# Kernel tuning notes

Measured on AMD Instinct MI355X. Metric: run time of the kernel, lower is better.

Reference implementation:

```python
import jax, jax.numpy as jnp
import numpy as np

N, M, H = 65536, 256, 4           # memory_units, memory_unit_size, num_heads
CTRL, IN, OUT = 1024, 2048, 2048  # ctrl_dim, input_dim, output_dim
LSTM_IN = IN + H * M
EPS = 1e-8


def setup_inputs() -> dict:
    key = jax.random.key(0)
    ks = jax.random.split(key, 12)
    s = 0.02
    return {
        "x": jax.random.normal(ks[0], (1, IN), jnp.float32),
        "prev_reads": jax.random.normal(ks[1], (H, M), jnp.float32),
        "prev_h": jax.random.normal(ks[2], (1, CTRL), jnp.float32),
        "prev_c": jax.random.normal(ks[3], (1, CTRL), jnp.float32),
        "memory": jax.random.normal(ks[4], (N, M), jnp.float32) * 0.1,
        "prev_rw": jax.nn.softmax(jax.random.normal(ks[5], (H, N), jnp.float32), axis=-1),
        "prev_ww": jax.nn.softmax(jax.random.normal(ks[6], (H, N), jnp.float32), axis=-1),
        "W_ih": jax.random.normal(ks[7], (4 * CTRL, LSTM_IN), jnp.float32) * s,
        "W_hh": jax.random.normal(ks[8], (4 * CTRL, CTRL), jnp.float32) * s,
        "b_lstm": jnp.zeros((4 * CTRL,), jnp.float32),
        "W_out": jax.random.normal(ks[9], (OUT, H * M), jnp.float32) * s,
        "b_out": jnp.zeros((OUT,), jnp.float32),
        "Ww": jax.random.normal(ks[10], (H, 3 * M + 6, CTRL), jnp.float32) * s,
        "bw": jnp.zeros((H, 3 * M + 6), jnp.float32),
        "Wr": jax.random.normal(ks[11], (H, M + 6, CTRL), jnp.float32) * s,
        "br": jnp.zeros((H, M + 6), jnp.float32),
    }


def _address(o, prev_w, mem):
    # o: [M+6 or 3M+6] head fc output; prev_w: [N]; mem: [N, M]
    k = jnp.tanh(o[:M])                         # key
    beta = jax.nn.softplus(o[M])                # key strength
    g = jax.nn.sigmoid(o[M + 1])                # interpolation gate
    sft = jax.nn.softmax(o[M + 2:M + 5])        # shift weights (-1, 0, +1)
    gamma = 1.0 + jax.nn.softplus(o[M + 5])     # sharpening
    sim = (mem @ k) / (jnp.linalg.norm(mem, axis=1) * jnp.linalg.norm(k) + EPS)
    wc = jax.nn.softmax(beta * sim)             # content addressing [N]
    wg = g * wc + (1.0 - g) * prev_w            # interpolation
    ws = sft[0] * jnp.roll(wg, -1) + sft[1] * wg + sft[2] * jnp.roll(wg, 1)
    wsh = jnp.maximum(ws, 1e-12) ** gamma       # sharpen
    return wsh / (jnp.sum(wsh) + EPS)


def reference(x, prev_reads, prev_h, prev_c, memory, prev_rw, prev_ww,
              W_ih, W_hh, b_lstm, W_out, b_out, Ww, bw, Wr, br):
    # Controller LSTM cell: input = [x ; flattened previous reads]
    inp = jnp.concatenate([x, prev_reads.reshape(1, -1)], axis=-1)
    gates = inp @ W_ih.T + prev_h @ W_hh.T + b_lstm
    i_g, f_g, g_g, _ = jnp.split(gates, 4, axis=-1)
    c = jax.nn.sigmoid(f_g) * prev_c + jax.nn.sigmoid(i_g) * jnp.tanh(g_g)
    ctrl = c[0]  # heads consume the controller cell state (as in forward)
    mem = memory
    reads = []
    for hd in range(H):  # heads ordered [w0, r0, w1, r1, ...] as in the module
        ow = Ww[hd] @ ctrl + bw[hd]
        ww = _address(ow, prev_ww[hd], mem)
        e = jax.nn.sigmoid(ow[M + 6:2 * M + 6])
        a = jnp.tanh(ow[2 * M + 6:3 * M + 6])
        mem = mem * (1.0 - ww[:, None] * e[None, :]) + ww[:, None] * a[None, :]
        orr = Wr[hd] @ ctrl + br[hd]
        rw = _address(orr, prev_rw[hd], mem)
        reads.append(rw @ mem)  # [M]
    reads = jnp.stack(reads)    # [H, M]
    return reads.reshape(1, -1) @ W_out.T + b_out  # [1, OUT]
```

## Files before the change

kernel.cpp:

```cpp
#include <hip/hip_runtime.h>
#include <cmath>

#define NMEM 65536
#define MSZ  256
#define EPSC 1e-8f
#define GRID_BIG 512

enum : int {
    OFF_GATES = 0,
    OFF_CTRL  = 4096,
    OFF_OW    = 5120,
    OFF_ORR   = 8216,
    OFF_K     = 9264,
    OFF_E     = 11312,
    OFF_A     = 12336,
    OFF_SCAL  = 13360,
    OFF_READS = 13424,
    OFF_PAIRS = 14448,
    OFF_TPART = 15472,
    OFF_SIM   = 15728,
    OFF_WSH   = 81264,
    OFF_NSQ   = 146800,
    WS_FLOATS = 212336
};

__device__ __forceinline__ float wave_sum(float v) {
#pragma unroll
    for (int off = 32; off > 0; off >>= 1) v += __shfl_xor(v, off);
    return v;
}
__device__ __forceinline__ float sigmoidf_(float x) { return 1.f / (1.f + expf(-x)); }
__device__ __forceinline__ float softplusf_(float x) { return (x > 20.f) ? x : log1pf(expf(x)); }
__device__ __forceinline__ void pair_merge(float& m, float& s, float m2, float s2) {
    if (m2 > m) { s = s * expf(m - m2) + s2; m = m2; }
    else        { s += s2 * expf(m2 - m); }
}
__device__ __forceinline__ float dot4(float4 a, float4 b) {
    return a.x * b.x + a.y * b.y + a.z * b.z + a.w * b.w;
}

__device__ __forceinline__ void block_pair_out(float m, float s, float* ws,
                                               int t, int lane, int wid) {
    __shared__ float sm[4], ss2[4];
    if (lane == 0) { sm[wid] = m; ss2[wid] = s; }
    __syncthreads();
    if (t == 0) {
        float M = sm[0], S = ss2[0];
#pragma unroll
        for (int i = 1; i < 4; ++i) pair_merge(M, S, sm[i], ss2[i]);
        ws[OFF_PAIRS + blockIdx.x * 2]     = M;
        ws[OFF_PAIRS + blockIdx.x * 2 + 1] = S;
    }
}

#define BFLY8(arr)                                            \
    _Pragma("unroll")                                         \
    for (int off = 32; off > 0; off >>= 1) {                  \
        _Pragma("unroll")                                     \
        for (int r = 0; r < 8; ++r) arr[r] += __shfl_xor(arr[r], off); \
    }

__global__ __launch_bounds__(256) void k_gates(
    const float* __restrict__ x, const float* __restrict__ prev_reads,
    const float* __restrict__ prev_h, const float* __restrict__ W_ih,
    const float* __restrict__ W_hh, const float* __restrict__ b_lstm,
    float* __restrict__ ws)
{
    const int row  = (blockIdx.x * 256 + threadIdx.x) >> 6;
    const int lane = threadIdx.x & 63;
    const float* wrow = W_ih + (size_t)row * 3072;
    float acc = 0.f;
#pragma unroll
    for (int j = lane * 4; j < 3072; j += 256) {
        float4 w4 = *(const float4*)(wrow + j);
        float4 v4 = (j < 2048) ? *(const float4*)(x + j)
                               : *(const float4*)(prev_reads + (j - 2048));
        acc += dot4(w4, v4);
    }
    const float* hrow = W_hh + (size_t)row * 1024;
#pragma unroll
    for (int j = lane * 4; j < 1024; j += 256) {
        acc += dot4(*(const float4*)(hrow + j), *(const float4*)(prev_h + j));
    }
    acc = wave_sum(acc);
    if (lane == 0) ws[OFF_GATES + row] = acc + b_lstm[row];
}

__global__ void k_cell(const float* __restrict__ prev_c, float* __restrict__ ws) {
    const int j = blockIdx.x * blockDim.x + threadIdx.x;
    if (j >= 1024) return;
    const float ig = ws[OFF_GATES + j];
    const float fg = ws[OFF_GATES + 1024 + j];
    const float gg = ws[OFF_GATES + 2048 + j];
    ws[OFF_CTRL + j] = sigmoidf_(fg) * prev_c[j] + sigmoidf_(ig) * tanhf(gg);
}

__global__ __launch_bounds__(256) void k_headfc(
    const float* __restrict__ Ww, const float* __restrict__ bw,
    const float* __restrict__ Wr, const float* __restrict__ br,
    float* __restrict__ ws)
{
    const int gwv  = (blockIdx.x * 256 + threadIdx.x) >> 6;
    const int lane = threadIdx.x & 63;
    const float* wrow; float bias; int dst;
    if (gwv < 3096) { wrow = Ww + (size_t)gwv * 1024; bias = bw[gwv]; dst = OFF_OW + gwv; }
    else { const int rr = gwv - 3096; wrow = Wr + (size_t)rr * 1024; bias = br[rr]; dst = OFF_ORR + rr; }
    const float* ctrl = ws + OFF_CTRL;
    float acc = 0.f;
#pragma unroll
    for (int j = lane * 4; j < 1024; j += 256) {
        acc += dot4(*(const float4*)(wrow + j), *(const float4*)(ctrl + j));
    }
    acc = wave_sum(acc);
    if (lane == 0) ws[dst] = acc + bias;
}

__global__ __launch_bounds__(256) void k_params(float* __restrict__ ws) {
    const int p = blockIdx.x, t = threadIdx.x;
    const float* o = (p < 4) ? (ws + OFF_OW + p * 774) : (ws + OFF_ORR + (p - 4) * 262);
    const float kj = tanhf(o[t]);
    ws[OFF_K + p * 256 + t] = kj;
    float ssq = wave_sum(kj * kj);
    __shared__ float red[4];
    if ((t & 63) == 0) red[t >> 6] = ssq;
    __syncthreads();
    if (t == 0) {
        float* sc = ws + OFF_SCAL + p * 8;
        sc[0] = sqrtf(red[0] + red[1] + red[2] + red[3]);
        sc[1] = softplusf_(o[256]);
        sc[2] = sigmoidf_(o[257]);
        const float a0 = o[258], a1 = o[259], a2 = o[260];
        const float mm = fmaxf(a0, fmaxf(a1, a2));
        const float e0 = expf(a0 - mm), e1 = expf(a1 - mm), e2 = expf(a2 - mm);
        const float inv = 1.f / (e0 + e1 + e2);
        sc[3] = e0 * inv; sc[4] = e1 * inv; sc[5] = e2 * inv;
        sc[6] = 1.f + softplusf_(o[261]);
    }
    if (p < 4) {
        ws[OFF_E + p * 256 + t] = sigmoidf_(o[262 + t]);
        ws[OFF_A + p * 256 + t] = tanhf(o[518 + t]);
        ws[OFF_READS + p * 256 + t] = 0.f;
    }
}

__global__ __launch_bounds__(256) void k_sim(const float* __restrict__ mem,
                                             float* __restrict__ ws, int p)
{
    const int t = threadIdx.x, lane = t & 63, wid = t >> 6;
    const float4 k4   = *(const float4*)(ws + OFF_K + p * 256 + lane * 4);
    const float knorm = ws[OFF_SCAL + p * 8 + 0];
    const float beta  = ws[OFF_SCAL + p * 8 + 1];
    float m = -INFINITY, s = 0.f;
#pragma unroll
    for (int b = 0; b < 4; ++b) {
        const int n0 = blockIdx.x * 128 + wid * 32 + b * 8;
        float4 v[8];
#pragma unroll
        for (int r = 0; r < 8; ++r) v[r] = *(const float4*)(mem + (size_t)(n0 + r) * MSZ + lane * 4);
        float d[8], q[8];
#pragma unroll
        for (int r = 0; r < 8; ++r) { d[r] = dot4(v[r], k4); q[r] = dot4(v[r], v[r]); }
        BFLY8(d); BFLY8(q);
        float z8[8];
#pragma unroll
        for (int r = 0; r < 8; ++r) {
            const float sim = d[r] / (sqrtf(q[r]) * knorm + EPSC);
            if (lane == r) ws[OFF_SIM + n0 + r] = sim;
            z8[r] = beta * sim;
        }
        float mb = z8[0];
#pragma unroll
        for (int r = 1; r < 8; ++r) mb = fmaxf(mb, z8[r]);
        float sb = 0.f;
#pragma unroll
        for (int r = 0; r < 8; ++r) sb += expf(z8[r] - mb);
        pair_merge(m, s, mb, sb);
    }
    block_pair_out(m, s, ws, t, lane, wid);
}

__global__ __launch_bounds__(256) void k_smax(const float* __restrict__ prev_w,
                                              float* __restrict__ ws, int p)
{
    const int t = threadIdx.x;
    float m = ws[OFF_PAIRS + 2 * t], s = ws[OFF_PAIRS + 2 * t + 1];
    pair_merge(m, s, ws[OFF_PAIRS + 2 * (t + 256)], ws[OFF_PAIRS + 2 * (t + 256) + 1]);
    __shared__ float sm[256], ss[256];
    sm[t] = m; ss[t] = s;
    __syncthreads();
    for (int str = 128; str > 0; str >>= 1) {
        if (t < str) {
            float mm = sm[t], sss = ss[t];
            pair_merge(mm, sss, sm[t + str], ss[t + str]);
            sm[t] = mm; ss[t] = sss;
        }
        __syncthreads();
    }
    const float M = sm[0], invS = 1.f / ss[0];
    const float* sc = ws + OFF_SCAL + p * 8;
    const float beta = sc[1], g = sc[2], s0 = sc[3], s1 = sc[4], s2 = sc[5], gam = sc[6];
    const float* sim = ws + OFF_SIM;
    const int n  = blockIdx.x * 256 + t;
    const int np = (n + 1) & (NMEM - 1);
    const int nm = (n + NMEM - 1) & (NMEM - 1);
    const float wg0 = g * expf(beta * sim[n]  - M) * invS + (1.f - g) * prev_w[n];
    const float wgp = g * expf(beta * sim[np] - M) * invS + (1.f - g) * prev_w[np];
    const float wgm = g * expf(beta * sim[nm] - M) * invS + (1.f - g) * prev_w[nm];
    const float wsn = s0 * wgp + s1 * wg0 + s2 * wgm;
    const float wsh = powf(fmaxf(wsn, 1e-12f), gam);
    ws[OFF_WSH + n] = wsh;
    float tsum = wave_sum(wsh);
    __shared__ float red[4];
    if ((t & 63) == 0) red[t >> 6] = tsum;
    __syncthreads();
    if (t == 0) ws[OFF_TPART + blockIdx.x] = red[0] + red[1] + red[2] + red[3];
}

__device__ __forceinline__ float load_invT(const float* __restrict__ ws,
                                           int t, int lane, int wid) {
    __shared__ float red[4];
    float v = wave_sum(ws[OFF_TPART + t]);
    if (lane == 0) red[wid] = v;
    __syncthreads();
    return 1.f / (red[0] + red[1] + red[2] + red[3] + EPSC);
}

__global__ __launch_bounds__(256) void k_update(float* __restrict__ mem,
                                                float* __restrict__ ws, int hd, int store_nsq)
{
    const int t = threadIdx.x, lane = t & 63, wid = t >> 6;
    const float invT = load_invT(ws, t, lane, wid);
    const int p = 4 + hd;
    const float4 k4   = *(const float4*)(ws + OFF_K + p * 256 + lane * 4);
    const float4 e4   = *(const float4*)(ws + OFF_E + hd * 256 + lane * 4);
    const float4 a4   = *(const float4*)(ws + OFF_A + hd * 256 + lane * 4);
    const float knorm = ws[OFF_SCAL + p * 8 + 0];
    const float beta  = ws[OFF_SCAL + p * 8 + 1];
    float m = -INFINITY, s = 0.f;
#pragma unroll
    for (int b = 0; b < 4; ++b) {
        const int n0 = blockIdx.x * 128 + wid * 32 + b * 8;
        float w8[8]; float4 v[8];
#pragma unroll
        for (int r = 0; r < 8; ++r) w8[r] = ws[OFF_WSH + n0 + r] * invT;
#pragma unroll
        for (int r = 0; r < 8; ++r) v[r] = *(const float4*)(mem + (size_t)(n0 + r) * MSZ + lane * 4);
#pragma unroll
        for (int r = 0; r < 8; ++r) {
            const float w = w8[r];
            v[r].x = v[r].x * (1.f - w * e4.x) + w * a4.x;
            v[r].y = v[r].y * (1.f - w * e4.y) + w * a4.y;
            v[r].z = v[r].z * (1.f - w * e4.z) + w * a4.z;
            v[r].w = v[r].w * (1.f - w * e4.w) + w * a4.w;
            *(float4*)(mem + (size_t)(n0 + r) * MSZ + lane * 4) = v[r];
        }
        float d[8], q[8];
#pragma unroll
        for (int r = 0; r < 8; ++r) { d[r] = dot4(v[r], k4); q[r] = dot4(v[r], v[r]); }
        BFLY8(d); BFLY8(q);
        float z8[8];
#pragma unroll
        for (int r = 0; r < 8; ++r) {
            const float sim = d[r] / (sqrtf(q[r]) * knorm + EPSC);
            if (lane == r) {
                ws[OFF_SIM + n0 + r] = sim;
                if (store_nsq) ws[OFF_NSQ + n0 + r] = q[r];
            }
            z8[r] = beta * sim;
        }
        float mb = z8[0];
#pragma unroll
        for (int r = 1; r < 8; ++r) mb = fmaxf(mb, z8[r]);
        float sb = 0.f;
#pragma unroll
        for (int r = 0; r < 8; ++r) sb += expf(z8[r] - mb);
        pair_merge(m, s, mb, sb);
    }
    block_pair_out(m, s, ws, t, lane, wid);
}

__global__ __launch_bounds__(256) void k_readout(const float* __restrict__ mem,
                                                 float* __restrict__ ws, int hd,
                                                 int pnext, int use_nsq)
{
    const int t = threadIdx.x, lane = t & 63, wid = t >> 6;
    const float invT = load_invT(ws, t, lane, wid);
    float4 k4 = make_float4(0.f, 0.f, 0.f, 0.f);
    float knorm = 1.f, beta = 0.f;
    if (pnext >= 0) {
        k4    = *(const float4*)(ws + OFF_K + pnext * 256 + lane * 4);
        knorm = ws[OFF_SCAL + pnext * 8 + 0];
        beta  = ws[OFF_SCAL + pnext * 8 + 1];
    }
    float m = -INFINITY, s = 0.f;
    float4 acc = make_float4(0.f, 0.f, 0.f, 0.f);
#pragma unroll
    for (int b = 0; b < 4; ++b) {
        const int n0 = blockIdx.x * 128 + wid * 32 + b * 8;
        float w8[8]; float4 v[8];
#pragma unroll
        for (int r = 0; r < 8; ++r) w8[r] = ws[OFF_WSH + n0 + r] * invT;
#pragma unroll
        for (int r = 0; r < 8; ++r) v[r] = *(const float4*)(mem + (size_t)(n0 + r) * MSZ + lane * 4);
#pragma unroll
        for (int r = 0; r < 8; ++r) {
            acc.x += w8[r] * v[r].x; acc.y += w8[r] * v[r].y;
            acc.z += w8[r] * v[r].z; acc.w += w8[r] * v[r].w;
        }
        if (pnext >= 0) {
            float d[8], q[8];
#pragma unroll
            for (int r = 0; r < 8; ++r) d[r] = dot4(v[r], k4);
            BFLY8(d);
            if (use_nsq) {
#pragma unroll
                for (int r = 0; r < 8; ++r) q[r] = ws[OFF_NSQ + n0 + r];
            } else {
#pragma unroll
                for (int r = 0; r < 8; ++r) q[r] = dot4(v[r], v[r]);
                BFLY8(q);
            }
            float z8[8];
#pragma unroll
            for (int r = 0; r < 8; ++r) {
                const float sim = d[r] / (sqrtf(q[r]) * knorm + EPSC);
                if (lane == r) ws[OFF_SIM + n0 + r] = sim;
                z8[r] = beta * sim;
            }
            float mb = z8[0];
#pragma unroll
            for (int r = 1; r < 8; ++r) mb = fmaxf(mb, z8[r]);
            float sb = 0.f;
#pragma unroll
            for (int r = 0; r < 8; ++r) sb += expf(z8[r] - mb);
            pair_merge(m, s, mb, sb);
        }
    }
    __shared__ float lacc[4][256];
    lacc[wid][lane * 4 + 0] = acc.x;
    lacc[wid][lane * 4 + 1] = acc.y;
    lacc[wid][lane * 4 + 2] = acc.z;
    lacc[wid][lane * 4 + 3] = acc.w;
    __syncthreads();
    {
        const float vv = lacc[0][t] + lacc[1][t] + lacc[2][t] + lacc[3][t];
        atomicAdd(ws + OFF_READS + hd * 256 + t, vv);
    }
    if (pnext >= 0) block_pair_out(m, s, ws, t, lane, wid);
}

__global__ __launch_bounds__(256) void k_out(const float* __restrict__ W_out,
                                             const float* __restrict__ b_out,
                                             const float* __restrict__ ws,
                                             float* __restrict__ out)
{
    const int row  = (blockIdx.x * 256 + threadIdx.x) >> 6;
    const int lane = threadIdx.x & 63;
    const float* wr    = W_out + (size_t)row * 1024;
    const float* reads = ws + OFF_READS;
    float acc = 0.f;
#pragma unroll
    for (int j = lane * 4; j < 1024; j += 256) {
        acc += dot4(*(const float4*)(wr + j), *(const float4*)(reads + j));
    }
    acc = wave_sum(acc);
    if (lane == 0) out[row] = acc + b_out[row];
}

extern "C" void kernel_launch(void* const* d_in, const int* in_sizes, int n_in,
                              void* d_out, int out_size, void* d_ws, size_t ws_size,
                              hipStream_t stream) {
    (void)in_sizes; (void)n_in; (void)out_size;
    const float* x          = (const float*)d_in[0];
    const float* prev_reads = (const float*)d_in[1];
    const float* prev_h     = (const float*)d_in[2];
    const float* prev_c     = (const float*)d_in[3];
    float*       memory     = (float*)d_in[4];
    const float* prev_rw    = (const float*)d_in[5];
    const float* prev_ww    = (const float*)d_in[6];
    const float* W_ih       = (const float*)d_in[7];
    const float* W_hh       = (const float*)d_in[8];
    const float* b_lstm     = (const float*)d_in[9];
    const float* W_out      = (const float*)d_in[10];
    const float* b_out      = (const float*)d_in[11];
    const float* Ww         = (const float*)d_in[12];
    const float* bw         = (const float*)d_in[13];
    const float* Wr         = (const float*)d_in[14];
    const float* br         = (const float*)d_in[15];
    float* out = (float*)d_out;
    float* ws  = (float*)d_ws;
    const int use_nsq = (ws_size >= (size_t)WS_FLOATS * sizeof(float)) ? 1 : 0;

    k_gates <<<1024, 256, 0, stream>>>(x, prev_reads, prev_h, W_ih, W_hh, b_lstm, ws);
    k_cell  <<<4,    256, 0, stream>>>(prev_c, ws);
    k_headfc<<<1036, 256, 0, stream>>>(Ww, bw, Wr, br, ws);
    k_params<<<8,    256, 0, stream>>>(ws);
    k_sim   <<<GRID_BIG, 256, 0, stream>>>(memory, ws, 0);
    for (int hd = 0; hd < 4; ++hd) {
        k_smax   <<<256,      256, 0, stream>>>(prev_ww + (size_t)hd * NMEM, ws, hd);
        k_update <<<GRID_BIG, 256, 0, stream>>>(memory, ws, hd, use_nsq);
        k_smax   <<<256,      256, 0, stream>>>(prev_rw + (size_t)hd * NMEM, ws, 4 + hd);
        k_readout<<<GRID_BIG, 256, 0, stream>>>(memory, ws, hd, (hd < 3) ? (hd + 1) : -1, use_nsq);
    }
    k_out<<<512, 256, 0, stream>>>(W_out, b_out, ws, out);
}
```

Baseline: 479.7 us.

## Double grid size and issue all memory-row loads up front in streaming kernels

```diff
diff --git a/kernel.cpp b/kernel.cpp
--- a/kernel.cpp
+++ b/kernel.cpp
@@ -4,7 +4,7 @@
 #define NMEM 65536
 #define MSZ  256
 #define EPSC 1e-8f
-#define GRID_BIG 512
+#define GRID_BIG 1024
 
 enum : int {
     OFF_GATES = 0,
@@ -17,11 +17,11 @@
     OFF_SCAL  = 13360,
     OFF_READS = 13424,
     OFF_PAIRS = 14448,
-    OFF_TPART = 15472,
-    OFF_SIM   = 15728,
-    OFF_WSH   = 81264,
-    OFF_NSQ   = 146800,
-    WS_FLOATS = 212336
+    OFF_TPART = 16496,
+    OFF_SIM   = 16752,
+    OFF_WSH   = 82288,
+    OFF_NSQ   = 147824,
+    WS_FLOATS = 213360
 };
 
 __device__ __forceinline__ float wave_sum(float v) {
@@ -58,6 +58,23 @@
     for (int off = 32; off > 0; off >>= 1) {                  \
         _Pragma("unroll")                                     \
         for (int r = 0; r < 8; ++r) arr[r] += __shfl_xor(arr[r], off); \
+    }
+
+#define SIM_EPILOGUE(d, q, n0, mb, sb)                        \
+    {                                                         \
+        float z8[8];                                          \
+        _Pragma("unroll")                                     \
+        for (int r = 0; r < 8; ++r) {                         \
+            const float sim = d[r] / (sqrtf(q[r]) * knorm + EPSC); \
+            if (lane == r) ws[OFF_SIM + (n0) + r] = sim;      \
+            z8[r] = beta * sim;                               \
+        }                                                     \
+        mb = z8[0];                                           \
+        _Pragma("unroll")                                     \
+        for (int r = 1; r < 8; ++r) mb = fmaxf(mb, z8[r]);    \
+        sb = 0.f;                                             \
+        _Pragma("unroll")                                     \
+        for (int r = 0; r < 8; ++r) sb += expf(z8[r] - mb);   \
     }
 
 __global__ __launch_bounds__(256) void k_gates(
@@ -150,33 +167,25 @@
     const float4 k4   = *(const float4*)(ws + OFF_K + p * 256 + lane * 4);
     const float knorm = ws[OFF_SCAL + p * 8 + 0];
     const float beta  = ws[OFF_SCAL + p * 8 + 1];
-    float m = -INFINITY, s = 0.f;
-#pragma unroll
-    for (int b = 0; b < 4; ++b) {
-        const int n0 = blockIdx.x * 128 + wid * 32 + b * 8;
-        float4 v[8];
-#pragma unroll
-        for (int r = 0; r < 8; ++r) v[r] = *(const float4*)(mem + (size_t)(n0 + r) * MSZ + lane * 4);
-        float d[8], q[8];
-#pragma unroll
-        for (int r = 0; r < 8; ++r) { d[r] = dot4(v[r], k4); q[r] = dot4(v[r], v[r]); }
-        BFLY8(d); BFLY8(q);
-        float z8[8];
-#pragma unroll
-        for (int r = 0; r < 8; ++r) {
-            const float sim = d[r] / (sqrtf(q[r]) * knorm + EPSC);
-            if (lane == r) ws[OFF_SIM + n0 + r] = sim;
-            z8[r] = beta * sim;
-        }
-        float mb = z8[0];
-#pragma unroll
-        for (int r = 1; r < 8; ++r) mb = fmaxf(mb, z8[r]);
-        float sb = 0.f;
-#pragma unroll
-        for (int r = 0; r < 8; ++r) sb += expf(z8[r] - mb);
-        pair_merge(m, s, mb, sb);
-    }
-    block_pair_out(m, s, ws, t, lane, wid);
+    const int nA = blockIdx.x * 64 + wid * 16;
+    const int nB = nA + 8;
+    float4 vA[8], vB[8];
+#pragma unroll
+    for (int r = 0; r < 8; ++r) vA[r] = *(const float4*)(mem + (size_t)(nA + r) * MSZ + lane * 4);
+#pragma unroll
+    for (int r = 0; r < 8; ++r) vB[r] = *(const float4*)(mem + (size_t)(nB + r) * MSZ + lane * 4);
+    float dA[8], qA[8];
+#pragma unroll
+    for (int r = 0; r < 8; ++r) { dA[r] = dot4(vA[r], k4); qA[r] = dot4(vA[r], vA[r]); }
+    BFLY8(dA); BFLY8(qA);
+    float mA, sA; SIM_EPILOGUE(dA, qA, nA, mA, sA);
+    float dB[8], qB[8];
+#pragma unroll
+    for (int r = 0; r < 8; ++r) { dB[r] = dot4(vB[r], k4); qB[r] = dot4(vB[r], vB[r]); }
+    BFLY8(dB); BFLY8(qB);
+    float mB, sB; SIM_EPILOGUE(dB, qB, nB, mB, sB);
+    pair_merge(mA, sA, mB, sB);
+    block_pair_out(mA, sA, ws, t, lane, wid);
 }
 
 __global__ __launch_bounds__(256) void k_smax(const float* __restrict__ prev_w,
@@ -184,7 +193,9 @@
 {
     const int t = threadIdx.x;
     float m = ws[OFF_PAIRS + 2 * t], s = ws[OFF_PAIRS + 2 * t + 1];
-    pair_merge(m, s, ws[OFF_PAIRS + 2 * (t + 256)], ws[OFF_PAIRS + 2 * (t + 256) + 1]);
+#pragma unroll
+    for (int b = 1; b < 4; ++b)
+        pair_merge(m, s, ws[OFF_PAIRS + 2 * (t + 256 * b)], ws[OFF_PAIRS + 2 * (t + 256 * b) + 1]);
     __shared__ float sm[256], ss[256];
     sm[t] = m; ss[t] = s;
     __syncthreads();
@@ -236,47 +247,55 @@
     const float4 a4   = *(const float4*)(ws + OFF_A + hd * 256 + lane * 4);
     const float knorm = ws[OFF_SCAL + p * 8 + 0];
     const float beta  = ws[OFF_SCAL + p * 8 + 1];
-    float m = -INFINITY, s = 0.f;
-#pragma unroll
-    for (int b = 0; b < 4; ++b) {
-        const int n0 = blockIdx.x * 128 + wid * 32 + b * 8;
-        float w8[8]; float4 v[8];
-#pragma unroll
-        for (int r = 0; r < 8; ++r) w8[r] = ws[OFF_WSH + n0 + r] * invT;
-#pragma unroll
-        for (int r = 0; r < 8; ++r) v[r] = *(const float4*)(mem + (size_t)(n0 + r) * MSZ + lane * 4);
-#pragma unroll
-        for (int r = 0; r < 8; ++r) {
-            const float w = w8[r];
-            v[r].x = v[r].x * (1.f - w * e4.x) + w * a4.x;
-            v[r].y = v[r].y * (1.f - w * e4.y) + w * a4.y;
-            v[r].z = v[r].z * (1.f - w * e4.z) + w * a4.z;
-            v[r].w = v[r].w * (1.f - w * e4.w) + w * a4.w;
-            *(float4*)(mem + (size_t)(n0 + r) * MSZ + lane * 4) = v[r];
-        }
-        float d[8], q[8];
-#pragma unroll
-        for (int r = 0; r < 8; ++r) { d[r] = dot4(v[r], k4); q[r] = dot4(v[r], v[r]); }
-        BFLY8(d); BFLY8(q);
-        float z8[8];
-#pragma unroll
-        for (int r = 0; r < 8; ++r) {
-            const float sim = d[r] / (sqrtf(q[r]) * knorm + EPSC);
-            if (lane == r) {
-                ws[OFF_SIM + n0 + r] = sim;
-                if (store_nsq) ws[OFF_NSQ + n0 + r] = q[r];
-            }
-            z8[r] = beta * sim;
-        }
-        float mb = z8[0];
-#pragma unroll
-        for (int r = 1; r < 8; ++r) mb = fmaxf(mb, z8[r]);
-        float sb = 0.f;
-#pragma unroll
-        for (int r = 0; r < 8; ++r) sb += expf(z8[r] - mb);
-        pair_merge(m, s, mb, sb);
-    }
-    block_pair_out(m, s, ws, t, lane, wid);
+    const int nA = blockIdx.x * 64 + wid * 16;
+    const int nB = nA + 8;
+    float wA[8], wB[8]; float4 vA[8], vB[8];
+#pragma unroll
+    for (int r = 0; r < 8; ++r) wA[r] = ws[OFF_WSH + nA + r];
+#pragma unroll
+    for (int r = 0; r < 8; ++r) wB[r] = ws[OFF_WSH + nB + r];
+#pragma unroll
+    for (int r = 0; r < 8; ++r) vA[r] = *(const float4*)(mem + (size_t)(nA + r) * MSZ + lane * 4);
+#pragma unroll
+    for (int r = 0; r < 8; ++r) vB[r] = *(const float4*)(mem + (size_t)(nB + r) * MSZ + lane * 4);
+#pragma unroll
+    for (int r = 0; r < 8; ++r) {
+        const float w = wA[r] * invT;
+        vA[r].x = vA[r].x * (1.f - w * e4.x) + w * a4.x;
+        vA[r].y = vA[r].y * (1.f - w * e4.y) + w * a4.y;
+        vA[r].z = vA[r].z * (1.f - w * e4.z) + w * a4.z;
+        vA[r].w = vA[r].w * (1.f - w * e4.w) + w * a4.w;
+        *(float4*)(mem + (size_t)(nA + r) * MSZ + lane * 4) = vA[r];
+    }
+#pragma unroll
+    for (int r = 0; r < 8; ++r) {
+        const float w = wB[r] * invT;
+        vB[r].x = vB[r].x * (1.f - w * e4.x) + w * a4.x;
+        vB[r].y = vB[r].y * (1.f - w * e4.y) + w * a4.y;
+        vB[r].z = vB[r].z * (1.f - w * e4.z) + w * a4.z;
+        vB[r].w = vB[r].w * (1.f - w * e4.w) + w * a4.w;
+        *(float4*)(mem + (size_t)(nB + r) * MSZ + lane * 4) = vB[r];
+    }
+    float dA[8], qA[8];
+#pragma unroll
+    for (int r = 0; r < 8; ++r) { dA[r] = dot4(vA[r], k4); qA[r] = dot4(vA[r], vA[r]); }
+    BFLY8(dA); BFLY8(qA);
+    if (store_nsq) {
+#pragma unroll
+        for (int r = 0; r < 8; ++r) if (lane == r) ws[OFF_NSQ + nA + r] = qA[r];
+    }
+    float mA, sA; SIM_EPILOGUE(dA, qA, nA, mA, sA);
+    float dB[8], qB[8];
+#pragma unroll
+    for (int r = 0; r < 8; ++r) { dB[r] = dot4(vB[r], k4); qB[r] = dot4(vB[r], vB[r]); }
+    BFLY8(dB); BFLY8(qB);
+    if (store_nsq) {
+#pragma unroll
+        for (int r = 0; r < 8; ++r) if (lane == r) ws[OFF_NSQ + nB + r] = qB[r];
+    }
+    float mB, sB; SIM_EPILOGUE(dB, qB, nB, mB, sB);
+    pair_merge(mA, sA, mB, sB);
+    block_pair_out(mA, sA, ws, t, lane, wid);
 }
 
 __global__ __launch_bounds__(256) void k_readout(const float* __restrict__ mem,
@@ -292,49 +311,60 @@
         knorm = ws[OFF_SCAL + pnext * 8 + 0];
         beta  = ws[OFF_SCAL + pnext * 8 + 1];
     }
+    const int nA = blockIdx.x * 64 + wid * 16;
+    const int nB = nA + 8;
+    float wA[8], wB[8]; float4 vA[8], vB[8];
+#pragma unroll
+    for (int r = 0; r < 8; ++r) wA[r] = ws[OFF_WSH + nA + r];
+#pragma unroll
+    for (int r = 0; r < 8; ++r) wB[r] = ws[OFF_WSH + nB + r];
+#pragma unroll
+    for (int r = 0; r < 8; ++r) vA[r] = *(const float4*)(mem + (size_t)(nA + r) * MSZ + lane * 4);
+#pragma unroll
+    for (int r = 0; r < 8; ++r) vB[r] = *(const float4*)(mem + (size_t)(nB + r) * MSZ + lane * 4);
+    float4 acc = make_float4(0.f, 0.f, 0.f, 0.f);
+#pragma unroll
+    for (int r = 0; r < 8; ++r) {
+        const float w = wA[r] * invT;
+        acc.x += w * vA[r].x; acc.y += w * vA[r].y;
+        acc.z += w * vA[r].z; acc.w += w * vA[r].w;
+    }
+#pragma unroll
+    for (int r = 0; r < 8; ++r) {
+        const float w = wB[r] * invT;
+        acc.x += w * vB[r].x; acc.y += w * vB[r].y;
+        acc.z += w * vB[r].z; acc.w += w * vB[r].w;
+    }
     float m = -INFINITY, s = 0.f;
-    float4 acc = make_float4(0.f, 0.f, 0.f, 0.f);
-#pragma unroll
-    for (int b = 0; b < 4; ++b) {
-        const int n0 = blockIdx.x * 128 + wid * 32 + b * 8;
-        float w8[8]; float4 v[8];
-#pragma unroll
-        for (int r = 0; r < 8; ++r) w8[r] = ws[OFF_WSH + n0 + r] * invT;
-#pragma unroll
-        for (int r = 0; r < 8; ++r) v[r] = *(const float4*)(mem + (size_t)(n0 + r) * MSZ + lane * 4);
-#pragma unroll
-        for (int r = 0; r < 8; ++r) {
-            acc.x += w8[r] * v[r].x; acc.y += w8[r] * v[r].y;
-            acc.z += w8[r] * v[r].z; acc.w += w8[r] * v[r].w;
+    if (pnext >= 0) {
+        float dA[8], qA[8];
+#pragma unroll
+        for (int r = 0; r < 8; ++r) dA[r] = dot4(vA[r], k4);
+        BFLY8(dA);
+        if (use_nsq) {
+#pragma unroll
+            for (int r = 0; r < 8; ++r) qA[r] = ws[OFF_NSQ + nA + r];
+        } else {
+#pragma unroll
+            for (int r = 0; r < 8; ++r) qA[r] = dot4(vA[r], vA[r]);
+            BFLY8(qA);
         }
-        if (pnext >= 0) {
-            float d[8], q[8];
-#pragma unroll
-            for (int r = 0; r < 8; ++r) d[r] = dot4(v[r], k4);
-            BFLY8(d);
-            if (use_nsq) {
-#pragma unroll
-                for (int r = 0; r < 8; ++r) q[r] = ws[OFF_NSQ + n0 + r];
-            } else {
-#pragma unroll
-                for (int r = 0; r < 8; ++r) q[r] = dot4(v[r], v[r]);
-                BFLY8(q);
-            }
-            float z8[8];
-#pragma unroll
-            for (int r = 0; r < 8; ++r) {
-                const float sim = d[r] / (sqrtf(q[r]) * knorm + EPSC);
-                if (lane == r) ws[OFF_SIM + n0 + r] = sim;
-                z8[r] = beta * sim;
-            }
-            float mb = z8[0];
-#pragma unroll
-            for (int r = 1; r < 8; ++r) mb = fmaxf(mb, z8[r]);
-            float sb = 0.f;
-#pragma unroll
-            for (int r = 0; r < 8; ++r) sb += expf(z8[r] - mb);
-            pair_merge(m, s, mb, sb);
+        float mA, sA; SIM_EPILOGUE(dA, qA, nA, mA, sA);
+        float dB[8], qB[8];
+#pragma unroll
+        for (int r = 0; r < 8; ++r) dB[r] = dot4(vB[r], k4);
+        BFLY8(dB);
+        if (use_nsq) {
+#pragma unroll
+            for (int r = 0; r < 8; ++r) qB[r] = ws[OFF_NSQ + nB + r];
+        } else {
+#pragma unroll
+            for (int r = 0; r < 8; ++r) qB[r] = dot4(vB[r], vB[r]);
+            BFLY8(qB);
         }
+        float mB, sB; SIM_EPILOGUE(dB, qB, nB, mB, sB);
+        pair_merge(mA, sA, mB, sB);
+        m = mA; s = sA;
     }
     __shared__ float lacc[4][256];
     lacc[wid][lane * 4 + 0] = acc.x;
```

Result: slower. 532.6 us (+11.0%).
